# Optimization experiments

Measured on AMD Instinct MI355X. Metric: run time of the kernel, lower is better.

## Reference

```python
import jax, jax.numpy as jnp
import numpy as np

N = 100000   # nodes
E = 1600000  # edges
D_IN, H1, H2, H3 = 128, 128, 128, 64


def _sage_layer(x, src, dst, Wl, Wr, b):
    # PyG SAGEConv (aggr='mean'): out = lin_l(mean_{j in N(i)} x_j) + lin_r(x_i)
    msg_sum = jax.ops.segment_sum(x[src], dst, num_segments=N)          # [N, F]
    deg = jax.ops.segment_sum(jnp.ones((src.shape[0],), x.dtype), dst, num_segments=N)
    mean = msg_sum / jnp.clip(deg, 1.0)[:, None]
    return mean @ Wl + x @ Wr + b


def setup_inputs() -> dict:
    key = jax.random.key(0)
    ks = jax.random.split(key, 11)
    x = jax.random.normal(ks[0], (N, D_IN), dtype=jnp.float32)
    edge_index = jax.random.randint(ks[1], (2, E), 0, N, dtype=jnp.int32)

    def w(k, fin, fout):
        return jax.random.normal(k, (fin, fout), dtype=jnp.float32) * (1.0 / np.sqrt(fin))

    return {
        "x": x,
        "edge_index": edge_index,
        "W1_l": w(ks[2], D_IN, H1), "W1_r": w(ks[3], D_IN, H1), "b1": jnp.zeros((H1,), jnp.float32),
        "W2_l": w(ks[4], H1, H2),  "W2_r": w(ks[5], H1, H2),  "b2": jnp.zeros((H2,), jnp.float32),
        "W3_l": w(ks[6], H2, H3),  "W3_r": w(ks[7], H2, H3),  "b3": jnp.zeros((H3,), jnp.float32),
    }


def reference(x, edge_index, W1_l, W1_r, b1, W2_l, W2_r, b2, W3_l, W3_r, b3):
    src, dst = edge_index[0], edge_index[1]
    h = jax.nn.relu(_sage_layer(x, src, dst, W1_l, W1_r, b1))
    h = jax.nn.relu(_sage_layer(h, src, dst, W2_l, W2_r, b2))
    return _sage_layer(h, src, dst, W3_l, W3_r, b3)
```

## Files before the change

### kernel.cpp

```cpp
#include <hip/hip_runtime.h>

#define NN 100000
#define NE 1600000
#define NPB 256
#define NB 391
#define CAP 4864
#define NBLK_A 512
#define CHUNK_A (NE / NBLK_A)

typedef __attribute__((ext_vector_type(8))) short bf16x8;
typedef __attribute__((ext_vector_type(4))) float f32x4;


__device__ __forceinline__ unsigned short f2bf(float f) {
    unsigned int u = __float_as_uint(f);
    unsigned int r = u + 0x7fffu + ((u >> 16) & 1u);
    return (unsigned short)(r >> 16);
}
__device__ __forceinline__ float bflo(unsigned int u) { return __uint_as_float(u << 16); }
__device__ __forceinline__ float bfhi(unsigned int u) { return __uint_as_float(u & 0xffff0000u); }
__device__ __forceinline__ unsigned int packbf(float lo, float hi) {
    return ((unsigned int)f2bf(hi) << 16) | (unsigned int)f2bf(lo);
}
__device__ __forceinline__ bf16x8 as_bf8(uint4 u) {
    union { uint4 u; bf16x8 h; } c;
    c.u = u;
    return c.h;
}


__global__ __launch_bounds__(256) void bucket_scatter_kernel(
    const int* __restrict__ src, const int* __restrict__ dst,
    int* __restrict__ gcur, uint2* __restrict__ buckets) {
    __shared__ int hist[NB];
    __shared__ int base[NB];
    int t = threadIdx.x;
    for (int b = t; b < NB; b += 256) hist[b] = 0;
    __syncthreads();
    int e0 = blockIdx.x * CHUNK_A;
    for (int e = e0 + t; e < e0 + CHUNK_A; e += 256)
        atomicAdd(&hist[dst[e] >> 8], 1);
    __syncthreads();
    for (int b = t; b < NB; b += 256) {
        base[b] = atomicAdd(&gcur[b], hist[b]);
        hist[b] = 0;
    }
    __syncthreads();
    for (int e = e0 + t; e < e0 + CHUNK_A; e += 256) {
        int d = dst[e];
        int bkt = d >> 8;
        int slot = base[bkt] + atomicAdd(&hist[bkt], 1);
        if (slot < CAP)
            buckets[(size_t)bkt * CAP + slot] = make_uint2((unsigned)src[e], (unsigned)d);
    }
}


__global__ void bucket_scan_kernel(const int* __restrict__ gcur, int* __restrict__ bstart,
                                   int* __restrict__ row_ptr) {
    if (blockIdx.x == 0 && threadIdx.x == 0) {
        int run = 0;
        for (int b = 0; b < NB; ++b) {
            bstart[b] = run;
            run += gcur[b];
        }
        bstart[NB] = run;
        row_ptr[NN] = run;
    }
}


__global__ __launch_bounds__(256) void csr_finalize_kernel(
    const uint2* __restrict__ buckets, const int* __restrict__ gcur,
    const int* __restrict__ bstart, int* __restrict__ row_ptr, int* __restrict__ adj) {
    __shared__ int hist[NPB];
    __shared__ int scn[NPB];
    int b = blockIdx.x;
    int t = threadIdx.x;
    int n = gcur[b];
    if (n > CAP) n = CAP;
    int base = bstart[b];
    const uint2* bk = buckets + (size_t)b * CAP;

    hist[t] = 0;
    __syncthreads();
    for (int i = t; i < n; i += 256) atomicAdd(&hist[bk[i].y & 255], 1);
    __syncthreads();

    int v = hist[t];
    scn[t] = v;
    __syncthreads();
    for (int off = 1; off < 256; off <<= 1) {
        int add = (t >= off) ? scn[t - off] : 0;
        __syncthreads();
        scn[t] += add;
        __syncthreads();
    }
    int excl = scn[t] - v;
    int node = b * NPB + t;
    if (node < NN) row_ptr[node] = base + excl;

    hist[t] = excl;
    __syncthreads();
    for (int i = t; i < n; i += 256) {
        uint2 pr = bk[i];
        int pos = atomicAdd(&hist[pr.y & 255], 1);
        adj[base + pos] = (int)pr.x;
    }
}


__global__ __launch_bounds__(256) void f32_to_bf16_kernel(const float* __restrict__ in,
                                                          unsigned int* __restrict__ outb,
                                                          int n8) {
    int i = blockIdx.x * blockDim.x + threadIdx.x;
    if (i >= n8) return;
    const float4* p = (const float4*)in + (size_t)i * 2;
    float4 a = p[0], b = p[1];
    uint4 r;
    r.x = packbf(a.x, a.y);
    r.y = packbf(a.z, a.w);
    r.z = packbf(b.x, b.y);
    r.w = packbf(b.z, b.w);
    ((uint4*)outb)[i] = r;
}


__device__ __forceinline__ void wfrag_one(const float* __restrict__ W, int H, int idx,
                                          uint4* __restrict__ out) {
    int lane = idx & 63;
    int tile = idx >> 6;
    int ntiles = H >> 4;
    int nt = tile % ntiles;
    int kt = tile / ntiles;
    int kbase = kt * 32 + (lane >> 4) * 8;
    int col = nt * 16 + (lane & 15);
    uint4 r;
    r.x = packbf(W[(size_t)(kbase + 0) * H + col], W[(size_t)(kbase + 1) * H + col]);
    r.y = packbf(W[(size_t)(kbase + 2) * H + col], W[(size_t)(kbase + 3) * H + col]);
    r.z = packbf(W[(size_t)(kbase + 4) * H + col], W[(size_t)(kbase + 5) * H + col]);
    r.w = packbf(W[(size_t)(kbase + 6) * H + col], W[(size_t)(kbase + 7) * H + col]);
    out[idx] = r;
}

__global__ __launch_bounds__(256) void wfrag_all_kernel(
    const float* __restrict__ W1l, const float* __restrict__ W1r,
    const float* __restrict__ W2l, const float* __restrict__ W2r,
    const float* __restrict__ W3l, const float* __restrict__ W3r,
    uint4* __restrict__ wf1, uint4* __restrict__ wf2,
    uint4* __restrict__ wf3l, uint4* __restrict__ wf3r) {
    int idx = blockIdx.x * blockDim.x + threadIdx.x;
    if (idx < 2048)       wfrag_one(W1l, 128, idx, wf1);
    else if (idx < 4096)  wfrag_one(W1r, 128, idx - 2048, wf1 + 2048);
    else if (idx < 6144)  wfrag_one(W2l, 128, idx - 4096, wf2);
    else if (idx < 8192)  wfrag_one(W2r, 128, idx - 6144, wf2 + 2048);
    else if (idx < 9216)  wfrag_one(W3l, 64, idx - 8192, wf3l);
    else if (idx < 10240) wfrag_one(W3r, 64, idx - 9216, wf3r);
}


__global__ __launch_bounds__(256) void pull_mean128_bf_kernel(
    const uint4* __restrict__ xb4, const int* __restrict__ row_ptr,
    const int* __restrict__ adj, uint4* __restrict__ aggb4) {
    int node = blockIdx.x * 4 + (threadIdx.x >> 6);
    int l = threadIdx.x & 63;
    int g = l >> 4;
    int i = l & 15;
    int beg = row_ptr[node], end = row_ptr[node + 1];
    float acc[8];
#pragma unroll
    for (int j = 0; j < 8; ++j) acc[j] = 0.f;

    for (int base = beg; base < end; base += 16) {
        uint4 u[4];
        float m[4];
#pragma unroll
        for (int j = 0; j < 4; ++j) {
            int e = base + j * 4 + g;
            bool v = e < end;
            int s = v ? adj[e] : 0;
            u[j] = xb4[(size_t)s * 16 + i];
            m[j] = v ? 1.f : 0.f;
        }
#pragma unroll
        for (int j = 0; j < 4; ++j) {
            acc[0] = fmaf(m[j], bflo(u[j].x), acc[0]);
            acc[1] = fmaf(m[j], bfhi(u[j].x), acc[1]);
            acc[2] = fmaf(m[j], bflo(u[j].y), acc[2]);
            acc[3] = fmaf(m[j], bfhi(u[j].y), acc[3]);
            acc[4] = fmaf(m[j], bflo(u[j].z), acc[4]);
            acc[5] = fmaf(m[j], bfhi(u[j].z), acc[5]);
            acc[6] = fmaf(m[j], bflo(u[j].w), acc[6]);
            acc[7] = fmaf(m[j], bfhi(u[j].w), acc[7]);
        }
    }

#pragma unroll
    for (int j = 0; j < 8; ++j) {
        acc[j] += __shfl_xor(acc[j], 16);
        acc[j] += __shfl_xor(acc[j], 32);
    }
    if (g == 0) {
        float inv = 1.0f / (float)(end > beg ? (end - beg) : 1);
        uint4 r;
        r.x = packbf(acc[0] * inv, acc[1] * inv);
        r.y = packbf(acc[2] * inv, acc[3] * inv);
        r.z = packbf(acc[4] * inv, acc[5] * inv);
        r.w = packbf(acc[6] * inv, acc[7] * inv);
        aggb4[(size_t)node * 16 + i] = r;
    }
}

__global__ __launch_bounds__(256) void pull_mean64_bf_kernel(
    const uint2* __restrict__ zb2, const int* __restrict__ row_ptr,
    const int* __restrict__ adj, float* __restrict__ aggout) {
    int node = blockIdx.x * 4 + (threadIdx.x >> 6);
    int l = threadIdx.x & 63;
    int g = l >> 4;
    int i = l & 15;
    int beg = row_ptr[node], end = row_ptr[node + 1];
    float acc[4];
#pragma unroll
    for (int j = 0; j < 4; ++j) acc[j] = 0.f;

    for (int base = beg; base < end; base += 16) {
        uint2 u[4];
        float m[4];
#pragma unroll
        for (int j = 0; j < 4; ++j) {
            int e = base + j * 4 + g;
            bool v = e < end;
            int s = v ? adj[e] : 0;
            u[j] = zb2[(size_t)s * 16 + i];
            m[j] = v ? 1.f : 0.f;
        }
#pragma unroll
        for (int j = 0; j < 4; ++j) {
            acc[0] = fmaf(m[j], bflo(u[j].x), acc[0]);
            acc[1] = fmaf(m[j], bfhi(u[j].x), acc[1]);
            acc[2] = fmaf(m[j], bflo(u[j].y), acc[2]);
            acc[3] = fmaf(m[j], bfhi(u[j].y), acc[3]);
        }
    }

#pragma unroll
    for (int j = 0; j < 4; ++j) {
        acc[j] += __shfl_xor(acc[j], 16);
        acc[j] += __shfl_xor(acc[j], 32);
    }
    if (g == 0) {
        float inv = 1.0f / (float)(end > beg ? (end - beg) : 1);
        float4 r;
        r.x = acc[0] * inv;
        r.y = acc[1] * inv;
        r.z = acc[2] * inv;
        r.w = acc[3] * inv;
        *(float4*)(aggout + (size_t)node * 64 + i * 4) = r;
    }
}


__global__ __launch_bounds__(256) void sage_mfma_kernel(
    const uint4* __restrict__ aggA, const uint4* __restrict__ xinA,
    const uint4* __restrict__ wfrag, const float* __restrict__ bias,
    unsigned short* __restrict__ outb) {
    const int w = threadIdx.x >> 6;
    const int l = threadIdx.x & 63;
    const int r0 = blockIdx.x * 64 + w * 16;
    int arow = r0 + (l & 15);
    if (arow > NN - 1) arow = NN - 1;
    const int koff = l >> 4;

    f32x4 acc[8];
#pragma unroll
    for (int nt = 0; nt < 8; ++nt) {
        f32x4 z = {0.f, 0.f, 0.f, 0.f};
        acc[nt] = z;
    }

#pragma unroll
    for (int kt = 0; kt < 8; ++kt) {
        const uint4* Ab = (kt < 4) ? aggA : xinA;
        const int ktl = kt & 3;
        bf16x8 av = as_bf8(Ab[(size_t)arow * 16 + ktl * 4 + koff]);
#pragma unroll
        for (int nt = 0; nt < 8; ++nt) {
            bf16x8 bv = as_bf8(wfrag[(kt * 8 + nt) * 64 + l]);
            acc[nt] = __builtin_amdgcn_mfma_f32_16x16x32_bf16(av, bv, acc[nt], 0, 0, 0);
        }
    }

    const int crow0 = r0 + ((l >> 4) << 2);
    const int ccol = l & 15;
#pragma unroll
    for (int nt = 0; nt < 8; ++nt) {
        float bb = bias[nt * 16 + ccol];
#pragma unroll
        for (int i = 0; i < 4; ++i) {
            int r = crow0 + i;
            if (r < NN) {
                float v = fmaxf(acc[nt][i] + bb, 0.f);
                outb[(size_t)r * 128 + nt * 16 + ccol] = f2bf(v);
            }
        }
    }
}


template <int MODE>
__global__ __launch_bounds__(256) void mm64_mfma_kernel(
    const uint4* __restrict__ A, const uint4* __restrict__ wfrag,
    const float* __restrict__ addin, const float* __restrict__ bias,
    void* __restrict__ outp) {
    const int w = threadIdx.x >> 6;
    const int l = threadIdx.x & 63;
    const int r0 = blockIdx.x * 64 + w * 16;
    int arow = r0 + (l & 15);
    if (arow > NN - 1) arow = NN - 1;
    const int koff = l >> 4;

    f32x4 acc[4];
#pragma unroll
    for (int nt = 0; nt < 4; ++nt) {
        f32x4 z = {0.f, 0.f, 0.f, 0.f};
        acc[nt] = z;
    }

#pragma unroll
    for (int kt = 0; kt < 4; ++kt) {
        bf16x8 av = as_bf8(A[(size_t)arow * 16 + kt * 4 + koff]);
#pragma unroll
        for (int nt = 0; nt < 4; ++nt) {
            bf16x8 bv = as_bf8(wfrag[(kt * 4 + nt) * 64 + l]);
            acc[nt] = __builtin_amdgcn_mfma_f32_16x16x32_bf16(av, bv, acc[nt], 0, 0, 0);
        }
    }

    const int crow0 = r0 + ((l >> 4) << 2);
    const int ccol = l & 15;
#pragma unroll
    for (int nt = 0; nt < 4; ++nt) {
        int col = nt * 16 + ccol;
#pragma unroll
        for (int i = 0; i < 4; ++i) {
            int r = crow0 + i;
            if (r < NN) {
                if (MODE == 0) {
                    ((unsigned short*)outp)[(size_t)r * 64 + col] = f2bf(acc[nt][i]);
                } else {
                    float v = acc[nt][i] + addin[(size_t)r * 64 + col] + bias[col];
                    ((float*)outp)[(size_t)r * 64 + col] = v;
                }
            }
        }
    }
}


extern "C" void kernel_launch(void* const* d_in, const int* in_sizes, int n_in,
                              void* d_out, int out_size, void* d_ws, size_t ws_size,
                              hipStream_t stream) {
    (void)in_sizes; (void)n_in; (void)out_size; (void)ws_size;

    const float* x   = (const float*)d_in[0];
    const int* eidx  = (const int*)d_in[1];
    const int* src   = eidx;
    const int* dst   = eidx + NE;
    const float* W1l = (const float*)d_in[2];
    const float* W1r = (const float*)d_in[3];
    const float* b1  = (const float*)d_in[4];
    const float* W2l = (const float*)d_in[5];
    const float* W2r = (const float*)d_in[6];
    const float* b2  = (const float*)d_in[7];
    const float* W3l = (const float*)d_in[8];
    const float* W3r = (const float*)d_in[9];
    const float* b3  = (const float*)d_in[10];
    float* out = (float*)d_out;

    size_t off = 0;
    auto carve = [&](size_t bytes) -> void* {
        void* p = (char*)d_ws + off;
        off += (bytes + 255) & ~(size_t)255;
        return p;
    };
    int* gcur    = (int*)carve((size_t)NB * 4);
    int* bstart  = (int*)carve((size_t)(NB + 1) * 4);
    int* row_ptr = (int*)carve((size_t)(NN + 1) * 4);
    int* adj     = (int*)carve((size_t)NE * 4);
    uint2* buckets = (uint2*)carve((size_t)NB * CAP * 8);
    unsigned int* x_bf   = (unsigned int*)carve((size_t)NN * 64 * 4);
    unsigned int* agg_bf = (unsigned int*)carve((size_t)NN * 64 * 4);
    unsigned int* h1_bf  = (unsigned int*)carve((size_t)NN * 64 * 4);
    unsigned int* h2_bf  = (unsigned int*)carve((size_t)NN * 64 * 4);
    unsigned int* z_bf   = (unsigned int*)carve((size_t)NN * 32 * 4);
    float* agg3          = (float*)carve((size_t)NN * 64 * 4);
    uint4* wf1  = (uint4*)carve((size_t)8 * 8 * 64 * 16);
    uint4* wf2  = (uint4*)carve((size_t)8 * 8 * 64 * 16);
    uint4* wf3l = (uint4*)carve((size_t)4 * 4 * 64 * 16);
    uint4* wf3r = (uint4*)carve((size_t)4 * 4 * 64 * 16);

    const int mgrid = (NN + 63) / 64;
    const int pgrid = (NN + 3) / 4;
    const int cgrid = (NN * 16 + 255) / 256;

    hipMemsetAsync(gcur, 0, (size_t)NB * 4, stream);
    bucket_scatter_kernel<<<NBLK_A, 256, 0, stream>>>(src, dst, gcur, buckets);
    bucket_scan_kernel<<<1, 64, 0, stream>>>(gcur, bstart, row_ptr);
    csr_finalize_kernel<<<NB, 256, 0, stream>>>(buckets, gcur, bstart, row_ptr, adj);

    f32_to_bf16_kernel<<<cgrid, 256, 0, stream>>>(x, x_bf, NN * 16);
    wfrag_all_kernel<<<40, 256, 0, stream>>>(W1l, W1r, W2l, W2r, W3l, W3r, wf1, wf2, wf3l, wf3r);

    pull_mean128_bf_kernel<<<pgrid, 256, 0, stream>>>((const uint4*)x_bf, row_ptr, adj, (uint4*)agg_bf);
    sage_mfma_kernel<<<mgrid, 256, 0, stream>>>((const uint4*)agg_bf, (const uint4*)x_bf,
                                                wf1, b1, (unsigned short*)h1_bf);
    pull_mean128_bf_kernel<<<pgrid, 256, 0, stream>>>((const uint4*)h1_bf, row_ptr, adj, (uint4*)agg_bf);
    sage_mfma_kernel<<<mgrid, 256, 0, stream>>>((const uint4*)agg_bf, (const uint4*)h1_bf,
                                                wf2, b2, (unsigned short*)h2_bf);
    mm64_mfma_kernel<0><<<mgrid, 256, 0, stream>>>((const uint4*)h2_bf, wf3l, nullptr, nullptr, z_bf);
    pull_mean64_bf_kernel<<<pgrid, 256, 0, stream>>>((const uint2*)z_bf, row_ptr, adj, agg3);
    mm64_mfma_kernel<1><<<mgrid, 256, 0, stream>>>((const uint4*)h2_bf, wf3r, agg3, b3, out);
}
```

Measured before the change: 340.2 us.

## Fuse neighbor mean aggregation into MFMA layer kernels and pack bucket entries

Each SAGE layer now gathers neighbor means into shared memory inside the same kernel that runs the MFMA matmul. This removes the agg_bf/agg3 intermediate round trips through global memory and several launches. Bucket entries are packed into a single 32-bit word (local dst in the high byte, src in the low 24 bits), and the bucket scan becomes a parallel block scan. The x conversion and weight fragment prep are merged into one launch. The trade-off is that each wave now processes 16 nodes serially in the gather phase with far fewer blocks, which may reduce latency hiding for the random gathers.

```diff
diff --git a/kernel.cpp b/kernel.cpp
--- a/kernel.cpp
+++ b/kernel.cpp
@@ -7,6 +7,7 @@
 #define CAP 4864
 #define NBLK_A 512
 #define CHUNK_A (NE / NBLK_A)
+#define CVT_N (NN * 16)
 
 typedef __attribute__((ext_vector_type(8))) short bf16x8;
 typedef __attribute__((ext_vector_type(4))) float f32x4;
@@ -31,7 +32,7 @@
 
 __global__ __launch_bounds__(256) void bucket_scatter_kernel(
     const int* __restrict__ src, const int* __restrict__ dst,
-    int* __restrict__ gcur, uint2* __restrict__ buckets) {
+    int* __restrict__ gcur, unsigned* __restrict__ buckets) {
     __shared__ int hist[NB];
     __shared__ int base[NB];
     int t = threadIdx.x;
@@ -51,27 +52,35 @@
         int bkt = d >> 8;
         int slot = base[bkt] + atomicAdd(&hist[bkt], 1);
         if (slot < CAP)
-            buckets[(size_t)bkt * CAP + slot] = make_uint2((unsigned)src[e], (unsigned)d);
-    }
-}
-
-
-__global__ void bucket_scan_kernel(const int* __restrict__ gcur, int* __restrict__ bstart,
-                                   int* __restrict__ row_ptr) {
-    if (blockIdx.x == 0 && threadIdx.x == 0) {
-        int run = 0;
-        for (int b = 0; b < NB; ++b) {
-            bstart[b] = run;
-            run += gcur[b];
-        }
-        bstart[NB] = run;
-        row_ptr[NN] = run;
+            buckets[(size_t)bkt * CAP + slot] =
+                ((unsigned)(d & 255) << 24) | (unsigned)src[e];
+    }
+}
+
+
+__global__ __launch_bounds__(512) void bucket_scan_kernel(
+    const int* __restrict__ gcur, int* __restrict__ bstart, int* __restrict__ row_ptr) {
+    __shared__ int s[512];
+    int t = threadIdx.x;
+    int v = (t < NB) ? gcur[t] : 0;
+    s[t] = v;
+    __syncthreads();
+    for (int off = 1; off < 512; off <<= 1) {
+        int a = (t >= off) ? s[t - off] : 0;
+        __syncthreads();
+        s[t] += a;
+        __syncthreads();
+    }
+    if (t < NB) bstart[t] = s[t] - v;
+    if (t == NB - 1) {
+        bstart[NB] = s[t];
+        row_ptr[NN] = s[t];
     }
 }
 
 
 __global__ __launch_bounds__(256) void csr_finalize_kernel(
-    const uint2* __restrict__ buckets, const int* __restrict__ gcur,
+    const unsigned* __restrict__ buckets, const int* __restrict__ gcur,
     const int* __restrict__ bstart, int* __restrict__ row_ptr, int* __restrict__ adj) {
     __shared__ int hist[NPB];
     __shared__ int scn[NPB];
@@ -80,11 +89,11 @@
     int n = gcur[b];
     if (n > CAP) n = CAP;
     int base = bstart[b];
-    const uint2* bk = buckets + (size_t)b * CAP;
+    const unsigned* bk = buckets + (size_t)b * CAP;
 
     hist[t] = 0;
     __syncthreads();
-    for (int i = t; i < n; i += 256) atomicAdd(&hist[bk[i].y & 255], 1);
+    for (int i = t; i < n; i += 256) atomicAdd(&hist[bk[i] >> 24], 1);
     __syncthreads();
 
     int v = hist[t];
@@ -103,26 +112,10 @@
     hist[t] = excl;
     __syncthreads();
     for (int i = t; i < n; i += 256) {
-        uint2 pr = bk[i];
-        int pos = atomicAdd(&hist[pr.y & 255], 1);
-        adj[base + pos] = (int)pr.x;
-    }
-}
-
-
-__global__ __launch_bounds__(256) void f32_to_bf16_kernel(const float* __restrict__ in,
-                                                          unsigned int* __restrict__ outb,
-                                                          int n8) {
-    int i = blockIdx.x * blockDim.x + threadIdx.x;
-    if (i >= n8) return;
-    const float4* p = (const float4*)in + (size_t)i * 2;
-    float4 a = p[0], b = p[1];
-    uint4 r;
-    r.x = packbf(a.x, a.y);
-    r.y = packbf(a.z, a.w);
-    r.z = packbf(b.x, b.y);
-    r.w = packbf(b.z, b.w);
-    ((uint4*)outb)[i] = r;
+        unsigned pr = bk[i];
+        int pos = atomicAdd(&hist[pr >> 24], 1);
+        adj[base + pos] = (int)(pr & 0xFFFFFFu);
+    }
 }
 
 
@@ -143,126 +136,156 @@
     out[idx] = r;
 }
 
-__global__ __launch_bounds__(256) void wfrag_all_kernel(
+__global__ __launch_bounds__(256) void prep_kernel(
+    const float* __restrict__ x, unsigned int* __restrict__ x_bf,
     const float* __restrict__ W1l, const float* __restrict__ W1r,
     const float* __restrict__ W2l, const float* __restrict__ W2r,
     const float* __restrict__ W3l, const float* __restrict__ W3r,
     uint4* __restrict__ wf1, uint4* __restrict__ wf2,
     uint4* __restrict__ wf3l, uint4* __restrict__ wf3r) {
     int idx = blockIdx.x * blockDim.x + threadIdx.x;
-    if (idx < 2048)       wfrag_one(W1l, 128, idx, wf1);
-    else if (idx < 4096)  wfrag_one(W1r, 128, idx - 2048, wf1 + 2048);
-    else if (idx < 6144)  wfrag_one(W2l, 128, idx - 4096, wf2);
-    else if (idx < 8192)  wfrag_one(W2r, 128, idx - 6144, wf2 + 2048);
-    else if (idx < 9216)  wfrag_one(W3l, 64, idx - 8192, wf3l);
-    else if (idx < 10240) wfrag_one(W3r, 64, idx - 9216, wf3r);
-}
-
-
-__global__ __launch_bounds__(256) void pull_mean128_bf_kernel(
+    if (idx < CVT_N) {
+        const float4* p = (const float4*)x + (size_t)idx * 2;
+        float4 a = p[0], b = p[1];
+        uint4 r;
+        r.x = packbf(a.x, a.y);
+        r.y = packbf(a.z, a.w);
+        r.z = packbf(b.x, b.y);
+        r.w = packbf(b.z, b.w);
+        ((uint4*)x_bf)[idx] = r;
+    } else {
+        int k = idx - CVT_N;
+        if (k < 2048)       wfrag_one(W1l, 128, k, wf1);
+        else if (k < 4096)  wfrag_one(W1r, 128, k - 2048, wf1 + 2048);
+        else if (k < 6144)  wfrag_one(W2l, 128, k - 4096, wf2);
+        else if (k < 8192)  wfrag_one(W2r, 128, k - 6144, wf2 + 2048);
+        else if (k < 9216)  wfrag_one(W3l, 64, k - 8192, wf3l);
+        else if (k < 10240) wfrag_one(W3r, 64, k - 9216, wf3r);
+    }
+}
+
+
+__global__ __launch_bounds__(256) void sage_fused_kernel(
     const uint4* __restrict__ xb4, const int* __restrict__ row_ptr,
-    const int* __restrict__ adj, uint4* __restrict__ aggb4) {
-    int node = blockIdx.x * 4 + (threadIdx.x >> 6);
-    int l = threadIdx.x & 63;
-    int g = l >> 4;
-    int i = l & 15;
-    int beg = row_ptr[node], end = row_ptr[node + 1];
-    float acc[8];
-#pragma unroll
-    for (int j = 0; j < 8; ++j) acc[j] = 0.f;
-
-    for (int base = beg; base < end; base += 16) {
-        uint4 u[4];
-        float m[4];
-#pragma unroll
-        for (int j = 0; j < 4; ++j) {
-            int e = base + j * 4 + g;
-            bool v = e < end;
-            int s = v ? adj[e] : 0;
-            u[j] = xb4[(size_t)s * 16 + i];
-            m[j] = v ? 1.f : 0.f;
-        }
-#pragma unroll
-        for (int j = 0; j < 4; ++j) {
-            acc[0] = fmaf(m[j], bflo(u[j].x), acc[0]);
-            acc[1] = fmaf(m[j], bfhi(u[j].x), acc[1]);
-            acc[2] = fmaf(m[j], bflo(u[j].y), acc[2]);
-            acc[3] = fmaf(m[j], bfhi(u[j].y), acc[3]);
-            acc[4] = fmaf(m[j], bflo(u[j].z), acc[4]);
-            acc[5] = fmaf(m[j], bfhi(u[j].z), acc[5]);
-            acc[6] = fmaf(m[j], bflo(u[j].w), acc[6]);
-            acc[7] = fmaf(m[j], bfhi(u[j].w), acc[7]);
-        }
-    }
-
-#pragma unroll
-    for (int j = 0; j < 8; ++j) {
-        acc[j] += __shfl_xor(acc[j], 16);
-        acc[j] += __shfl_xor(acc[j], 32);
-    }
-    if (g == 0) {
-        float inv = 1.0f / (float)(end > beg ? (end - beg) : 1);
-        uint4 r;
-        r.x = packbf(acc[0] * inv, acc[1] * inv);
-        r.y = packbf(acc[2] * inv, acc[3] * inv);
-        r.z = packbf(acc[4] * inv, acc[5] * inv);
-        r.w = packbf(acc[6] * inv, acc[7] * inv);
-        aggb4[(size_t)node * 16 + i] = r;
-    }
-}
-
-__global__ __launch_bounds__(256) void pull_mean64_bf_kernel(
-    const uint2* __restrict__ zb2, const int* __restrict__ row_ptr,
-    const int* __restrict__ adj, float* __restrict__ aggout) {
-    int node = blockIdx.x * 4 + (threadIdx.x >> 6);
-    int l = threadIdx.x & 63;
-    int g = l >> 4;
-    int i = l & 15;
-    int beg = row_ptr[node], end = row_ptr[node + 1];
-    float acc[4];
-#pragma unroll
-    for (int j = 0; j < 4; ++j) acc[j] = 0.f;
-
-    for (int base = beg; base < end; base += 16) {
-        uint2 u[4];
-        float m[4];
-#pragma unroll
-        for (int j = 0; j < 4; ++j) {
-            int e = base + j * 4 + g;
-            bool v = e < end;
-            int s = v ? adj[e] : 0;
-            u[j] = zb2[(size_t)s * 16 + i];
-            m[j] = v ? 1.f : 0.f;
-        }
-#pragma unroll
-        for (int j = 0; j < 4; ++j) {
-            acc[0] = fmaf(m[j], bflo(u[j].x), acc[0]);
-            acc[1] = fmaf(m[j], bfhi(u[j].x), acc[1]);
-            acc[2] = fmaf(m[j], bflo(u[j].y), acc[2]);
-            acc[3] = fmaf(m[j], bfhi(u[j].y), acc[3]);
-        }
-    }
-
-#pragma unroll
-    for (int j = 0; j < 4; ++j) {
-        acc[j] += __shfl_xor(acc[j], 16);
-        acc[j] += __shfl_xor(acc[j], 32);
-    }
-    if (g == 0) {
-        float inv = 1.0f / (float)(end > beg ? (end - beg) : 1);
-        float4 r;
-        r.x = acc[0] * inv;
-        r.y = acc[1] * inv;
-        r.z = acc[2] * inv;
-        r.w = acc[3] * inv;
-        *(float4*)(aggout + (size_t)node * 64 + i * 4) = r;
-    }
-}
-
-
-__global__ __launch_bounds__(256) void sage_mfma_kernel(
-    const uint4* __restrict__ aggA, const uint4* __restrict__ xinA,
-    const uint4* __restrict__ wfrag, const float* __restrict__ bias,
+    const int* __restrict__ adj, const uint4* __restrict__ wfrag,
+    const float* __restrict__ bias, unsigned short* __restrict__ outb) {
+    __shared__ uint4 As[64][17];
+
+    const int w = threadIdx.x >> 6;
+    const int l = threadIdx.x & 63;
+    const int g = l >> 4;
+    const int i = l & 15;
+    const int r0 = blockIdx.x * 64 + w * 16;
+
+    for (int wnode = 0; wnode < 16; ++wnode) {
+        int node = r0 + wnode;
+        float acc[8];
+#pragma unroll
+        for (int j = 0; j < 8; ++j) acc[j] = 0.f;
+        int beg = 0, end = 0;
+        if (node < NN) {
+            beg = row_ptr[node];
+            end = row_ptr[node + 1];
+        }
+        int p = beg;
+        for (; p + 16 <= end; p += 16) {
+#pragma unroll
+            for (int j = 0; j < 4; ++j) {
+                int s = adj[p + j * 4 + g];
+                uint4 u = xb4[(size_t)s * 16 + i];
+                acc[0] += bflo(u.x);
+                acc[1] += bfhi(u.x);
+                acc[2] += bflo(u.y);
+                acc[3] += bfhi(u.y);
+                acc[4] += bflo(u.z);
+                acc[5] += bfhi(u.z);
+                acc[6] += bflo(u.w);
+                acc[7] += bfhi(u.w);
+            }
+        }
+        if (p < end) {
+#pragma unroll
+            for (int j = 0; j < 4; ++j) {
+                int e = p + j * 4 + g;
+                bool vv = e < end;
+                int s = vv ? adj[e] : 0;
+                uint4 u = xb4[(size_t)s * 16 + i];
+                float m = vv ? 1.f : 0.f;
+                acc[0] = fmaf(m, bflo(u.x), acc[0]);
+                acc[1] = fmaf(m, bfhi(u.x), acc[1]);
+                acc[2] = fmaf(m, bflo(u.y), acc[2]);
+                acc[3] = fmaf(m, bfhi(u.y), acc[3]);
+                acc[4] = fmaf(m, bflo(u.z), acc[4]);
+                acc[5] = fmaf(m, bfhi(u.z), acc[5]);
+                acc[6] = fmaf(m, bflo(u.w), acc[6]);
+                acc[7] = fmaf(m, bfhi(u.w), acc[7]);
+            }
+        }
+#pragma unroll
+        for (int j = 0; j < 8; ++j) {
+            acc[j] += __shfl_xor(acc[j], 16);
+            acc[j] += __shfl_xor(acc[j], 32);
+        }
+        if (g == 0) {
+            float inv = 1.0f / (float)(end > beg ? (end - beg) : 1);
+            uint4 r;
+            r.x = packbf(acc[0] * inv, acc[1] * inv);
+            r.y = packbf(acc[2] * inv, acc[3] * inv);
+            r.z = packbf(acc[4] * inv, acc[5] * inv);
+            r.w = packbf(acc[6] * inv, acc[7] * inv);
+            As[w * 16 + wnode][i] = r;
+        }
+    }
+
+    const int koff = g;
+    int arow = r0 + (l & 15);
+    if (arow > NN - 1) arow = NN - 1;
+
+    f32x4 acc[8];
+#pragma unroll
+    for (int nt = 0; nt < 8; ++nt) {
+        f32x4 z = {0.f, 0.f, 0.f, 0.f};
+        acc[nt] = z;
+    }
+
+#pragma unroll
+    for (int kt = 0; kt < 4; ++kt) {
+        bf16x8 av = as_bf8(As[w * 16 + (l & 15)][kt * 4 + koff]);
+#pragma unroll
+        for (int nt = 0; nt < 8; ++nt) {
+            bf16x8 bv = as_bf8(wfrag[(kt * 8 + nt) * 64 + l]);
+            acc[nt] = __builtin_amdgcn_mfma_f32_16x16x32_bf16(av, bv, acc[nt], 0, 0, 0);
+        }
+    }
+#pragma unroll
+    for (int kt = 4; kt < 8; ++kt) {
+        bf16x8 av = as_bf8(xb4[(size_t)arow * 16 + (kt & 3) * 4 + koff]);
+#pragma unroll
+        for (int nt = 0; nt < 8; ++nt) {
+            bf16x8 bv = as_bf8(wfrag[(kt * 8 + nt) * 64 + l]);
+            acc[nt] = __builtin_amdgcn_mfma_f32_16x16x32_bf16(av, bv, acc[nt], 0, 0, 0);
+        }
+    }
+
+    const int crow0 = r0 + ((l >> 4) << 2);
+    const int ccol = l & 15;
+#pragma unroll
+    for (int nt = 0; nt < 8; ++nt) {
+        float bb = bias[nt * 16 + ccol];
+#pragma unroll
+        for (int q = 0; q < 4; ++q) {
+            int r = crow0 + q;
+            if (r < NN) {
+                float v = fmaxf(acc[nt][q] + bb, 0.f);
+                outb[(size_t)r * 128 + nt * 16 + ccol] = f2bf(v);
+            }
+        }
+    }
+}
+
+
+__global__ __launch_bounds__(256) void mm64_mfma_kernel(
+    const uint4* __restrict__ A, const uint4* __restrict__ wfrag,
     unsigned short* __restrict__ outb) {
     const int w = threadIdx.x >> 6;
     const int l = threadIdx.x & 63;
@@ -271,54 +294,6 @@
     if (arow > NN - 1) arow = NN - 1;
     const int koff = l >> 4;
 
-    f32x4 acc[8];
-#pragma unroll
-    for (int nt = 0; nt < 8; ++nt) {
-        f32x4 z = {0.f, 0.f, 0.f, 0.f};
-        acc[nt] = z;
-    }
-
-#pragma unroll
-    for (int kt = 0; kt < 8; ++kt) {
-        const uint4* Ab = (kt < 4) ? aggA : xinA;
-        const int ktl = kt & 3;
-        bf16x8 av = as_bf8(Ab[(size_t)arow * 16 + ktl * 4 + koff]);
-#pragma unroll
-        for (int nt = 0; nt < 8; ++nt) {
-            bf16x8 bv = as_bf8(wfrag[(kt * 8 + nt) * 64 + l]);
-            acc[nt] = __builtin_amdgcn_mfma_f32_16x16x32_bf16(av, bv, acc[nt], 0, 0, 0);
-        }
-    }
-
-    const int crow0 = r0 + ((l >> 4) << 2);
-    const int ccol = l & 15;
-#pragma unroll
-    for (int nt = 0; nt < 8; ++nt) {
-        float bb = bias[nt * 16 + ccol];
-#pragma unroll
-        for (int i = 0; i < 4; ++i) {
-            int r = crow0 + i;
-            if (r < NN) {
-                float v = fmaxf(acc[nt][i] + bb, 0.f);
-                outb[(size_t)r * 128 + nt * 16 + ccol] = f2bf(v);
-            }
-        }
-    }
-}
-
-
-template <int MODE>
-__global__ __launch_bounds__(256) void mm64_mfma_kernel(
-    const uint4* __restrict__ A, const uint4* __restrict__ wfrag,
-    const float* __restrict__ addin, const float* __restrict__ bias,
-    void* __restrict__ outp) {
-    const int w = threadIdx.x >> 6;
-    const int l = threadIdx.x & 63;
-    const int r0 = blockIdx.x * 64 + w * 16;
-    int arow = r0 + (l & 15);
-    if (arow > NN - 1) arow = NN - 1;
-    const int koff = l >> 4;
-
     f32x4 acc[4];
 #pragma unroll
     for (int nt = 0; nt < 4; ++nt) {
@@ -342,15 +317,112 @@
     for (int nt = 0; nt < 4; ++nt) {
         int col = nt * 16 + ccol;
 #pragma unroll
-        for (int i = 0; i < 4; ++i) {
-            int r = crow0 + i;
+        for (int q = 0; q < 4; ++q) {
+            int r = crow0 + q;
+            if (r < NN) outb[(size_t)r * 64 + col] = f2bf(acc[nt][q]);
+        }
+    }
+}
+
+
+__global__ __launch_bounds__(256) void final_fused_kernel(
+    const uint2* __restrict__ zb2, const int* __restrict__ row_ptr,
+    const int* __restrict__ adj, const uint4* __restrict__ h2A,
+    const uint4* __restrict__ wfrag, const float* __restrict__ bias,
+    float* __restrict__ out) {
+    __shared__ float As64[64][68];
+
+    const int w = threadIdx.x >> 6;
+    const int l = threadIdx.x & 63;
+    const int g = l >> 4;
+    const int i = l & 15;
+    const int r0 = blockIdx.x * 64 + w * 16;
+
+    for (int wnode = 0; wnode < 16; ++wnode) {
+        int node = r0 + wnode;
+        float acc[4];
+#pragma unroll
+        for (int j = 0; j < 4; ++j) acc[j] = 0.f;
+        int beg = 0, end = 0;
+        if (node < NN) {
+            beg = row_ptr[node];
+            end = row_ptr[node + 1];
+        }
+        int p = beg;
+        for (; p + 16 <= end; p += 16) {
+#pragma unroll
+            for (int j = 0; j < 4; ++j) {
+                int s = adj[p + j * 4 + g];
+                uint2 u = zb2[(size_t)s * 16 + i];
+                acc[0] += bflo(u.x);
+                acc[1] += bfhi(u.x);
+                acc[2] += bflo(u.y);
+                acc[3] += bfhi(u.y);
+            }
+        }
+        if (p < end) {
+#pragma unroll
+            for (int j = 0; j < 4; ++j) {
+                int e = p + j * 4 + g;
+                bool vv = e < end;
+                int s = vv ? adj[e] : 0;
+                uint2 u = zb2[(size_t)s * 16 + i];
+                float m = vv ? 1.f : 0.f;
+                acc[0] = fmaf(m, bflo(u.x), acc[0]);
+                acc[1] = fmaf(m, bfhi(u.x), acc[1]);
+                acc[2] = fmaf(m, bflo(u.y), acc[2]);
+                acc[3] = fmaf(m, bfhi(u.y), acc[3]);
+            }
+        }
+#pragma unroll
+        for (int j = 0; j < 4; ++j) {
+            acc[j] += __shfl_xor(acc[j], 16);
+            acc[j] += __shfl_xor(acc[j], 32);
+        }
+        if (g == 0) {
+            float inv = 1.0f / (float)(end > beg ? (end - beg) : 1);
+            float4 r;
+            r.x = acc[0] * inv;
+            r.y = acc[1] * inv;
+            r.z = acc[2] * inv;
+            r.w = acc[3] * inv;
+            *(float4*)(&As64[w * 16 + wnode][i * 4]) = r;
+        }
+    }
+
+    int arow = r0 + (l & 15);
+    if (arow > NN - 1) arow = NN - 1;
+    const int koff = g;
+
+    f32x4 acc[4];
+#pragma unroll
+    for (int nt = 0; nt < 4; ++nt) {
+        f32x4 z = {0.f, 0.f, 0.f, 0.f};
+        acc[nt] = z;
+    }
+
+#pragma unroll
+    for (int kt = 0; kt < 4; ++kt) {
+        bf16x8 av = as_bf8(h2A[(size_t)arow * 16 + kt * 4 + koff]);
+#pragma unroll
+        for (int nt = 0; nt < 4; ++nt) {
+            bf16x8 bv = as_bf8(wfrag[(kt * 4 + nt) * 64 + l]);
+            acc[nt] = __builtin_amdgcn_mfma_f32_16x16x32_bf16(av, bv, acc[nt], 0, 0, 0);
+        }
+    }
+
+    const int lrow0 = (l >> 4) << 2;
+    const int ccol = l & 15;
+#pragma unroll
+    for (int nt = 0; nt < 4; ++nt) {
+        int col = nt * 16 + ccol;
+        float bb = bias[col];
+#pragma unroll
+        for (int q = 0; q < 4; ++q) {
+            int r = r0 + lrow0 + q;
             if (r < NN) {
-                if (MODE == 0) {
-                    ((unsigned short*)outp)[(size_t)r * 64 + col] = f2bf(acc[nt][i]);
-                } else {
-                    float v = acc[nt][i] + addin[(size_t)r * 64 + col] + bias[col];
-                    ((float*)outp)[(size_t)r * 64 + col] = v;
-                }
+                float v = acc[nt][q] + As64[w * 16 + lrow0 + q][col] + bb;
+                out[(size_t)r * 64 + col] = v;
             }
         }
     }
@@ -387,37 +459,33 @@
     int* bstart  = (int*)carve((size_t)(NB + 1) * 4);
     int* row_ptr = (int*)carve((size_t)(NN + 1) * 4);
     int* adj     = (int*)carve((size_t)NE * 4);
-    uint2* buckets = (uint2*)carve((size_t)NB * CAP * 8);
-    unsigned int* x_bf   = (unsigned int*)carve((size_t)NN * 64 * 4);
-    unsigned int* agg_bf = (unsigned int*)carve((size_t)NN * 64 * 4);
-    unsigned int* h1_bf  = (unsigned int*)carve((size_t)NN * 64 * 4);
-    unsigned int* h2_bf  = (unsigned int*)carve((size_t)NN * 64 * 4);
-    unsigned int* z_bf   = (unsigned int*)carve((size_t)NN * 32 * 4);
-    float* agg3          = (float*)carve((size_t)NN * 64 * 4);
+    unsigned* buckets = (unsigned*)carve((size_t)NB * CAP * 4);
+    unsigned int* x_bf  = (unsigned int*)carve((size_t)NN * 64 * 4);
+    unsigned int* h1_bf = (unsigned int*)carve((size_t)NN * 64 * 4);
+    unsigned int* h2_bf = (unsigned int*)carve((size_t)NN * 64 * 4);
+    unsigned int* z_bf  = (unsigned int*)carve((size_t)NN * 32 * 4);
     uint4* wf1  = (uint4*)carve((size_t)8 * 8 * 64 * 16);
     uint4* wf2  = (uint4*)carve((size_t)8 * 8 * 64 * 16);
     uint4* wf3l = (uint4*)carve((size_t)4 * 4 * 64 * 16);
     uint4* wf3r = (uint4*)carve((size_t)4 * 4 * 64 * 16);
 
     const int mgrid = (NN + 63) / 64;
-    const int pgrid = (NN + 3) / 4;
-    const int cgrid = (NN * 16 + 255) / 256;
+    const int pgrid = (CVT_N + 10240 + 255) / 256;
 
     hipMemsetAsync(gcur, 0, (size_t)NB * 4, stream);
     bucket_scatter_kernel<<<NBLK_A, 256, 0, stream>>>(src, dst, gcur, buckets);
-    bucket_scan_kernel<<<1, 64, 0, stream>>>(gcur, bstart, row_ptr);
+    bucket_scan_kernel<<<1, 512, 0, stream>>>(gcur, bstart, row_ptr);
     csr_finalize_kernel<<<NB, 256, 0, stream>>>(buckets, gcur, bstart, row_ptr, adj);
 
-    f32_to_bf16_kernel<<<cgrid, 256, 0, stream>>>(x, x_bf, NN * 16);
-    wfrag_all_kernel<<<40, 256, 0, stream>>>(W1l, W1r, W2l, W2r, W3l, W3r, wf1, wf2, wf3l, wf3r);
-
-    pull_mean128_bf_kernel<<<pgrid, 256, 0, stream>>>((const uint4*)x_bf, row_ptr, adj, (uint4*)agg_bf);
-    sage_mfma_kernel<<<mgrid, 256, 0, stream>>>((const uint4*)agg_bf, (const uint4*)x_bf,
-                                                wf1, b1, (unsigned short*)h1_bf);
-    pull_mean128_bf_kernel<<<pgrid, 256, 0, stream>>>((const uint4*)h1_bf, row_ptr, adj, (uint4*)agg_bf);
-    sage_mfma_kernel<<<mgrid, 256, 0, stream>>>((const uint4*)agg_bf, (const uint4*)h1_bf,
-                                                wf2, b2, (unsigned short*)h2_bf);
-    mm64_mfma_kernel<0><<<mgrid, 256, 0, stream>>>((const uint4*)h2_bf, wf3l, nullptr, nullptr, z_bf);
-    pull_mean64_bf_kernel<<<pgrid, 256, 0, stream>>>((const uint2*)z_bf, row_ptr, adj, agg3);
-    mm64_mfma_kernel<1><<<mgrid, 256, 0, stream>>>((const uint4*)h2_bf, wf3r, agg3, b3, out);
-}
+    prep_kernel<<<pgrid, 256, 0, stream>>>(x, x_bf, W1l, W1r, W2l, W2r, W3l, W3r,
+                                           wf1, wf2, wf3l, wf3r);
+
+    sage_fused_kernel<<<mgrid, 256, 0, stream>>>((const uint4*)x_bf, row_ptr, adj,
+                                                 wf1, b1, (unsigned short*)h1_bf);
+    sage_fused_kernel<<<mgrid, 256, 0, stream>>>((const uint4*)h1_bf, row_ptr, adj,
+                                                 wf2, b2, (unsigned short*)h2_bf);
+    mm64_mfma_kernel<<<mgrid, 256, 0, stream>>>((const uint4*)h2_bf, wf3l,
+                                                (unsigned short*)z_bf);
+    final_fused_kernel<<<mgrid, 256, 0, stream>>>((const uint2*)z_bf, row_ptr, adj,
+                                                  (const uint4*)h2_bf, wf3r, b3, out);
+}
```

New measurement: 333.5 us. Within noise of the previous version (-2.0%).
